# Performance work log

Measured on AMD Instinct MI355X. Metric: run time of the kernel, lower is better.

The kernel has to match this reference:

```python
import jax, jax.numpy as jnp
import numpy as np

N, LATENT, HIDDEN, OUT, B = 65536, 128, 512, 64, 1024
W_WIDTH = 4.0  # LSH bucket width params['w']


def setup_inputs() -> dict:
    key = jax.random.key(0)
    ks = jax.random.split(key, 6)
    return {
        "z": jax.random.normal(ks[0], (N, LATENT), jnp.float32),
        "W1": jax.random.normal(ks[1], (LATENT, HIDDEN), jnp.float32) / np.float32(np.sqrt(LATENT)),
        "b1": jnp.zeros((HIDDEN,), jnp.float32),
        "W2": jax.random.normal(ks[2], (HIDDEN, OUT), jnp.float32) / np.float32(np.sqrt(HIDDEN)),
        "b2": jnp.zeros((OUT,), jnp.float32),
        "a": jax.random.normal(ks[3], (OUT,), jnp.float32),
        "lsh_b": jax.random.uniform(ks[4], (1,), jnp.float32) * W_WIDTH,
    }


def reference(z, W1, b1, W2, b2, a, lsh_b):
    # decoder MLP: latent -> hidden (relu) -> output_dim
    h = jax.nn.relu(z @ W1 + b1)
    x = h @ W2 + b2                                     # [N, OUT]
    # LSH random-projection hash: floor((x.a + b)/w), bucketed mod B
    code = jnp.floor((x @ a + lsh_b[0]) / W_WIDTH)
    bucket = jnp.mod(code.astype(jnp.int32), B)         # [N] segment ids
    # dict-based cluster grouping -> segmented mean per hash bucket
    sums = jax.ops.segment_sum(x, bucket, num_segments=B)                # [B, OUT]
    counts = jax.ops.segment_sum(jnp.ones((x.shape[0],), x.dtype), bucket, num_segments=B)
    means = sums / jnp.maximum(counts, 1.0)[:, None]    # [B, OUT]
    # squared distances point -> every cluster mean (gram trick, no [N,B,OUT] tensor)
    d2 = jnp.maximum(
        jnp.sum(x * x, -1)[:, None] + jnp.sum(means * means, -1)[None, :]
        - 2.0 * (x @ means.T),
        0.0)                                            # [N, B]
    # DEC-style Student-t soft cluster assignment
    q = 1.0 / (1.0 + d2)
    q_s = q / jnp.sum(q, -1, keepdims=True)
    return (q_s, means)
```

## Files before the change

kernel.cpp:

```cpp
#include <hip/hip_runtime.h>
#include <hip/hip_bf16.h>

#define N_PTS   65536
#define LATENT  128
#define HIDDEN  512
#define OUT_D   64
#define NBUCKET 1024
#define ROWS_A  32

typedef __attribute__((ext_vector_type(8))) short frag_ab;
typedef __attribute__((ext_vector_type(4))) float f32x4;

__device__ __forceinline__ short bf16h(float f) {
    union { float f; unsigned u; } c; c.f = f;
    const unsigned r = (c.u + 0x7FFFu + ((c.u >> 16) & 1u)) >> 16;
    return (short)r;
}
__device__ __forceinline__ float bf16tof(short s) {
    union { unsigned u; float f; } c; c.u = ((unsigned)(unsigned short)s) << 16;
    return c.f;
}
__device__ __forceinline__ float fbits(unsigned u) {
    union { unsigned u; float f; } c; c.u = u; return c.f;
}

__global__ __launch_bounds__(256) void prep_weights(
    const float* __restrict__ W1, const float* __restrict__ W2,
    short* __restrict__ w1frag, short* __restrict__ w2frag)
{
    const int tid = blockIdx.x * 256 + threadIdx.x;
    if (tid < 32 * 64 * 4) {
        const int ct = tid >> 8, l = (tid >> 2) & 63, ks = tid & 3;
        const int n = ct * 16 + (l & 15);
        const int k0 = ks * 32 + ((l >> 4) << 3);
        frag_ab hi, lo;
#pragma unroll
        for (int e = 0; e < 8; ++e) {
            const float wv = W1[(size_t)(k0 + e) * HIDDEN + n];
            const short h = bf16h(wv);
            hi[e] = h;
            lo[e] = bf16h(wv - bf16tof(h));
        }
        frag_ab* dst = (frag_ab*)w1frag;
        const int u = ((ct * 64 + l) * 4 + ks) * 2;
        dst[u] = hi; dst[u + 1] = lo;
    } else {
        const int u0 = tid - 32 * 64 * 4;
        const int c = u0 >> 8, ot = (u0 >> 6) & 3, l = u0 & 63;
        const int n = ot * 16 + (l & 15);
        frag_ab hi, lo;
#pragma unroll
        for (int e = 0; e < 8; ++e) {
            const int k = c * 32 + ((e >> 2) << 4) + ((l >> 4) << 2) + (e & 3);
            const float wv = W2[(size_t)k * OUT_D + n];
            const short h = bf16h(wv);
            hi[e] = h;
            lo[e] = bf16h(wv - bf16tof(h));
        }
        frag_ab* dst = (frag_ab*)w2frag;
        const int u = ((c * 4 + ot) * 64 + l) * 2;
        dst[u] = hi; dst[u + 1] = lo;
    }
}

#define WB_UNITS 1728
#define W2L_OFF  1152
#define XP_STRIDE 512
#define BAND_U   5e-4f

__global__ __launch_bounds__(256, 2) void mlp_mfma_kernel(
    const float* __restrict__ z, const short* __restrict__ w1frag,
    const short* __restrict__ w2frag, const float* __restrict__ b1,
    const float* __restrict__ b2, const float* __restrict__ a,
    const float* __restrict__ lsh_b,
    short* __restrict__ xhi, short* __restrict__ xlo,
    float* __restrict__ xnorm_out, int* __restrict__ bucket_out,
    int* __restrict__ wsflag)
{
    __shared__ frag_ab LD[2 * WB_UNITS];
    short* LDs = (short*)LD;
    const int t = threadIdx.x;
    const int l = t & 63, w = t >> 6;
    const int row0 = blockIdx.x * 128 + w * 32;

    frag_ab zh[2][4], zl[2][4];
#pragma unroll
    for (int rg = 0; rg < 2; ++rg)
#pragma unroll
        for (int ks = 0; ks < 4; ++ks) {
            const float* src = z + (size_t)(row0 + rg * 16 + (l & 15)) * LATENT
                             + ks * 32 + ((l >> 4) << 3);
            const float4 p0 = *(const float4*)src;
            const float4 p1 = *(const float4*)(src + 4);
            const float v[8] = {p0.x, p0.y, p0.z, p0.w, p1.x, p1.y, p1.z, p1.w};
#pragma unroll
            for (int e = 0; e < 8; ++e) {
                const short h = bf16h(v[e]);
                zh[rg][ks][e] = h;
                zl[rg][ks][e] = bf16h(v[e] - bf16tof(h));
            }
        }

    f32x4 acc2[2][4];
#pragma unroll
    for (int rg = 0; rg < 2; ++rg)
#pragma unroll
        for (int ot = 0; ot < 4; ++ot) acc2[rg][ot] = (f32x4){0.f, 0.f, 0.f, 0.f};

    const frag_ab* w1g = (const frag_ab*)w1frag;
    const frag_ab* w2g = (const frag_ab*)w2frag;

#pragma unroll
    for (int j = 0; j < 4; ++j) {
        const int i = t + 256 * j;
        LD[(i >> 9) * 576 + ((i >> 3) & 63) * 9 + (i & 7)] = w1g[i];
    }
#pragma unroll
    for (int j = 0; j < 2; ++j) {
        const int i = t + 256 * j;
        LD[W2L_OFF + ((i >> 1) & 63) * 9 + (((i >> 7) << 1) | (i & 1))] = w2g[i];
    }
    __syncthreads();

#pragma unroll 1
    for (int c = 0; c < 16; ++c) {
        const int pb = (c & 1) * WB_UNITS;
        const int sb = WB_UNITS - pb;
        frag_ab st1[4], st2[2];
        if (c < 15) {
#pragma unroll
            for (int j = 0; j < 4; ++j) st1[j] = w1g[(c + 1) * 1024 + t + 256 * j];
#pragma unroll
            for (int j = 0; j < 2; ++j) st2[j] = w2g[(c + 1) * 512 + t + 256 * j];
        }

        f32x4 acc1[2][2];
#pragma unroll
        for (int ct_l = 0; ct_l < 2; ++ct_l) {
            frag_ab bh[4], bl[4];
#pragma unroll
            for (int ks = 0; ks < 4; ++ks) {
                bh[ks] = LD[pb + ct_l * 576 + l * 9 + ks * 2];
                bl[ks] = LD[pb + ct_l * 576 + l * 9 + ks * 2 + 1];
            }
#pragma unroll
            for (int rg = 0; rg < 2; ++rg) {
                f32x4 acc = (f32x4){0.f, 0.f, 0.f, 0.f};
#pragma unroll
                for (int ks = 0; ks < 4; ++ks) {
                    acc = __builtin_amdgcn_mfma_f32_16x16x32_bf16(bh[ks], zh[rg][ks], acc, 0, 0, 0);
                    acc = __builtin_amdgcn_mfma_f32_16x16x32_bf16(bl[ks], zh[rg][ks], acc, 0, 0, 0);
                    acc = __builtin_amdgcn_mfma_f32_16x16x32_bf16(bh[ks], zl[rg][ks], acc, 0, 0, 0);
                }
                acc1[ct_l][rg] = acc;
            }
        }

        float4 b1v[2];
#pragma unroll
        for (int ct_l = 0; ct_l < 2; ++ct_l)
            b1v[ct_l] = *(const float4*)&b1[(c * 2 + ct_l) * 16 + ((l >> 4) << 2)];
        frag_ab ah2[2], al2[2];
#pragma unroll
        for (int rg = 0; rg < 2; ++rg)
#pragma unroll
            for (int e = 0; e < 8; ++e) {
                const int tile = e >> 2, r = e & 3;
                const float bb = (r == 0) ? b1v[tile].x : (r == 1) ? b1v[tile].y
                               : (r == 2) ? b1v[tile].z : b1v[tile].w;
                const float hv = fmaxf(acc1[tile][rg][r] + bb, 0.f);
                const short hh = bf16h(hv);
                ah2[rg][e] = hh;
                al2[rg][e] = bf16h(hv - bf16tof(hh));
            }

#pragma unroll
        for (int ot = 0; ot < 4; ++ot) {
            const frag_ab b2h = LD[pb + W2L_OFF + l * 9 + ot * 2];
            const frag_ab b2l = LD[pb + W2L_OFF + l * 9 + ot * 2 + 1];
#pragma unroll
            for (int rg = 0; rg < 2; ++rg) {
                acc2[rg][ot] = __builtin_amdgcn_mfma_f32_16x16x32_bf16(ah2[rg], b2h, acc2[rg][ot], 0, 0, 0);
                acc2[rg][ot] = __builtin_amdgcn_mfma_f32_16x16x32_bf16(al2[rg], b2h, acc2[rg][ot], 0, 0, 0);
                acc2[rg][ot] = __builtin_amdgcn_mfma_f32_16x16x32_bf16(ah2[rg], b2l, acc2[rg][ot], 0, 0, 0);
            }
        }

        if (c < 15) {
#pragma unroll
            for (int j = 0; j < 4; ++j) {
                const int i = t + 256 * j;
                LD[sb + (i >> 9) * 576 + ((i >> 3) & 63) * 9 + (i & 7)] = st1[j];
            }
#pragma unroll
            for (int j = 0; j < 2; ++j) {
                const int i = t + 256 * j;
                LD[sb + W2L_OFF + ((i >> 1) & 63) * 9 + (((i >> 7) << 1) | (i & 1))] = st2[j];
            }
        }
        __syncthreads();
    }
    __syncthreads();

    float b2v[4], av[4];
#pragma unroll
    for (int ot = 0; ot < 4; ++ot) {
        b2v[ot] = b2[ot * 16 + (l & 15)];
        av[ot]  = a[ot * 16 + (l & 15)];
    }
    const int pbase = w * XP_STRIDE;
    int flagged = 0;
    const float lb = lsh_b[0];
#pragma unroll
    for (int rg = 0; rg < 2; ++rg)
#pragma unroll
        for (int r = 0; r < 4; ++r) {
            float sp = 0.f, np = 0.f;
            const int row_l = rg * 16 + (l >> 4) * 4 + r;
#pragma unroll
            for (int ot = 0; ot < 4; ++ot) {
                const float xv = acc2[rg][ot][r] + b2v[ot];
                sp = fmaf(xv, av[ot], sp);
                np = fmaf(xv, xv, np);
                const int col = ot * 16 + (l & 15);
                const short xh = bf16h(xv);
                LDs[(pbase + row_l * 8 + (col >> 3)) * 8 + (col & 7)] = xh;
                LDs[(pbase + 256 + row_l * 8 + (col >> 3)) * 8 + (col & 7)] = bf16h(xv - bf16tof(xh));
            }
#pragma unroll
            for (int off = 8; off >= 1; off >>= 1) {
                sp += __shfl_xor(sp, off, 16);
                np += __shfl_xor(np, off, 16);
            }
            if ((l & 15) == 0) {
                const int row = row0 + row_l;
                const float v = sp + lb;
                const float u = v * 0.25f;
                const float fl = floorf(u);
                bucket_out[row] = ((int)fl) & (NBUCKET - 1);
                xnorm_out[row] = np;
                const float fr = u - fl;
                if (fr < BAND_U || fr > 1.f - BAND_U) flagged = 1;
            }
        }
    const unsigned long long fb = __ballot(flagged != 0);
    if (l == 0) wsflag[blockIdx.x * 4 + w] = (fb != 0ull) ? 1 : 0;

    frag_ab* xhi8 = (frag_ab*)xhi;
    frag_ab* xlo8 = (frag_ab*)xlo;
#pragma unroll
    for (int j = 0; j < 4; ++j) {
        const int u = l + 64 * j;
        const size_t gidx = (size_t)(row0 + (u >> 3)) * 8 + (u & 7);
        xhi8[gidx] = LD[pbase + u];
        xlo8[gidx] = LD[pbase + 256 + u];
    }
}

__global__ __launch_bounds__(256, 3) void mlp_fixup_kernel(
    const float* __restrict__ z, const float* __restrict__ W1,
    const float* __restrict__ b1, const float* __restrict__ W2,
    const float* __restrict__ b2, const float* __restrict__ a,
    const float* __restrict__ lsh_b, const int* __restrict__ wsflag,
    short* __restrict__ xhi, short* __restrict__ xlo,
    float* __restrict__ xnorm_out, int* __restrict__ bucket_out)
{
    if (wsflag[blockIdx.x] == 0) return;
    __shared__ float zt[ROWS_A][LATENT];
    __shared__ float ht[ROWS_A][256];
    const int t = threadIdx.x;
    const int row0 = blockIdx.x * ROWS_A;

    {
        const float4* z4 = reinterpret_cast<const float4*>(z + (size_t)row0 * LATENT);
        float4* zt4 = reinterpret_cast<float4*>(&zt[0][0]);
#pragma unroll
        for (int i = 0; i < 4; ++i) zt4[t + 256 * i] = z4[t + 256 * i];
    }
    __syncthreads();

    const int tx = t & 63, ty = t >> 6;
    const int txq = t & 31, tyq = t >> 5;

    float acc2[4][2];
#pragma unroll
    for (int i = 0; i < 4; ++i) { acc2[i][0] = 0.f; acc2[i][1] = 0.f; }

    for (int h = 0; h < 2; ++h) {
        float acc1[8][4];
#pragma unroll
        for (int i = 0; i < 8; ++i)
#pragma unroll
            for (int cc = 0; cc < 4; ++cc) acc1[i][cc] = 0.f;

        const int jbase = h * 256 + tx;
#pragma unroll 2
        for (int k = 0; k < LATENT; k += 4) {
            float wv[4][4];
#pragma unroll
            for (int kk = 0; kk < 4; ++kk)
#pragma unroll
                for (int cc = 0; cc < 4; ++cc)
                    wv[kk][cc] = W1[(size_t)(k + kk) * HIDDEN + jbase + 64 * cc];
            float4 zv[8];
#pragma unroll
            for (int i = 0; i < 8; ++i)
                zv[i] = *reinterpret_cast<const float4*>(&zt[ty * 8 + i][k]);
#pragma unroll
            for (int i = 0; i < 8; ++i)
#pragma unroll
                for (int cc = 0; cc < 4; ++cc) {
                    acc1[i][cc] = fmaf(zv[i].x, wv[0][cc], acc1[i][cc]);
                    acc1[i][cc] = fmaf(zv[i].y, wv[1][cc], acc1[i][cc]);
                    acc1[i][cc] = fmaf(zv[i].z, wv[2][cc], acc1[i][cc]);
                    acc1[i][cc] = fmaf(zv[i].w, wv[3][cc], acc1[i][cc]);
                }
        }
        float bb[4];
#pragma unroll
        for (int cc = 0; cc < 4; ++cc) bb[cc] = b1[jbase + 64 * cc];
#pragma unroll
        for (int i = 0; i < 8; ++i)
#pragma unroll
            for (int cc = 0; cc < 4; ++cc)
                ht[ty * 8 + i][tx + 64 * cc] = fmaxf(acc1[i][cc] + bb[cc], 0.f);
        __syncthreads();

#pragma unroll 2
        for (int k = 0; k < 256; k += 4) {
            float w2v[4][2];
#pragma unroll
            for (int kk = 0; kk < 4; ++kk) {
                w2v[kk][0] = W2[(size_t)(h * 256 + k + kk) * OUT_D + txq];
                w2v[kk][1] = W2[(size_t)(h * 256 + k + kk) * OUT_D + txq + 32];
            }
            float4 hv[4];
#pragma unroll
            for (int i = 0; i < 4; ++i)
                hv[i] = *reinterpret_cast<const float4*>(&ht[tyq * 4 + i][k]);
#pragma unroll
            for (int i = 0; i < 4; ++i)
#pragma unroll
                for (int cc = 0; cc < 2; ++cc) {
                    acc2[i][cc] = fmaf(hv[i].x, w2v[0][cc], acc2[i][cc]);
                    acc2[i][cc] = fmaf(hv[i].y, w2v[1][cc], acc2[i][cc]);
                    acc2[i][cc] = fmaf(hv[i].z, w2v[2][cc], acc2[i][cc]);
                    acc2[i][cc] = fmaf(hv[i].w, w2v[3][cc], acc2[i][cc]);
                }
        }
        __syncthreads();
    }

    const float bb0 = b2[txq], bb1 = b2[txq + 32];
    const float a0 = a[txq], a1 = a[txq + 32];
    const float lb = lsh_b[0];
#pragma unroll
    for (int i = 0; i < 4; ++i) {
        const int row = row0 + tyq * 4 + i;
        const float x0 = acc2[i][0] + bb0;
        const float x1 = acc2[i][1] + bb1;
        const short h0 = bf16h(x0), h1 = bf16h(x1);
        xhi[(size_t)row * OUT_D + txq]      = h0;
        xhi[(size_t)row * OUT_D + txq + 32] = h1;
        xlo[(size_t)row * OUT_D + txq]      = bf16h(x0 - bf16tof(h0));
        xlo[(size_t)row * OUT_D + txq + 32] = bf16h(x1 - bf16tof(h1));

        float sa = fmaf(x0, a0, x1 * a1);
        float sn = fmaf(x0, x0, x1 * x1);
#pragma unroll
        for (int off = 16; off >= 1; off >>= 1) {
            sa += __shfl_xor(sa, off, 32);
            sn += __shfl_xor(sn, off, 32);
        }
        if (txq == 0) {
            const float code = floorf((sa + lb) * 0.25f);
            bucket_out[row] = ((int)code) & (NBUCKET - 1);
            xnorm_out[row] = sn;
        }
    }
}

__global__ __launch_bounds__(256) void hist_kernel(
    const int* __restrict__ bucket, int* __restrict__ blockhist,
    float* __restrict__ sums)
{
    __shared__ int h[NBUCKET];
    const int t = threadIdx.x, blk = blockIdx.x;
    for (int i = t; i < NBUCKET; i += 256) h[i] = 0;
    for (int i = t; i < NBUCKET; i += 256) sums[blk * NBUCKET + i] = 0.f;
    __syncthreads();
    const int rbase = blk * 1024;
#pragma unroll
    for (int i = 0; i < 4; ++i)
        atomicAdd(&h[bucket[rbase + i * 256 + t]], 1);
    __syncthreads();
    for (int i = t; i < NBUCKET; i += 256)
        blockhist[blk * NBUCKET + i] = h[i];
}

__global__ __launch_bounds__(1024) void scan_kernel(
    const int* __restrict__ blockhist, int* __restrict__ base,
    int* __restrict__ blockbase)
{
    __shared__ int sc[NBUCKET];
    const int b = threadIdx.x;
    int c = 0;
#pragma unroll 8
    for (int blk = 0; blk < 64; ++blk) c += blockhist[blk * NBUCKET + b];
    sc[b] = c;
    __syncthreads();
    for (int off = 1; off < NBUCKET; off <<= 1) {
        const int add = (b >= off) ? sc[b - off] : 0;
        __syncthreads();
        sc[b] += add;
        __syncthreads();
    }
    const int offset = sc[b] - c;
    base[b] = offset;
    if (b == NBUCKET - 1) base[NBUCKET] = offset + c;
    int run = offset;
#pragma unroll 4
    for (int blk = 0; blk < 64; ++blk) {
        blockbase[blk * NBUCKET + b] = run;
        run += blockhist[blk * NBUCKET + b];
    }
}

__global__ __launch_bounds__(256) void scatter_kernel(
    const int* __restrict__ bucket, const int* __restrict__ blockbase,
    int* __restrict__ order)
{
    __shared__ int lcur[NBUCKET];
    const int t = threadIdx.x, blk = blockIdx.x;
    for (int i = t; i < NBUCKET; i += 256) lcur[i] = 0;
    __syncthreads();
    const int rbase = blk * 1024;
#pragma unroll
    for (int i = 0; i < 4; ++i) {
        const int row = rbase + i * 256 + t;
        const int bk = bucket[row];
        const int r = atomicAdd(&lcur[bk], 1);
        order[blockbase[blk * NBUCKET + bk] + r] = row;
    }
}

__global__ __launch_bounds__(256) void chunksum_kernel(
    const short* __restrict__ xhi, const short* __restrict__ xlo,
    const int* __restrict__ order, const int* __restrict__ bucket,
    float* __restrict__ sums)
{
    const int t = threadIdx.x, lane = t & 63, w = t >> 6;
    const int c = blockIdx.x * 4 + w;
    const int i0 = c * 64;
    const int ordv = order[i0 + lane];
    const int bktv = bucket[ordv];
    float acc = 0.f;
    int cur = __shfl(bktv, 0, 64);
#pragma unroll 8
    for (int j = 0; j < 64; ++j) {
        const int rb = __shfl(ordv, j, 64);
        const int bb = __shfl(bktv, j, 64);
        if (bb != cur) {
            atomicAdd(&sums[(size_t)cur * OUT_D + lane], acc);
            acc = 0.f; cur = bb;
        }
        acc += bf16tof(xhi[(size_t)rb * OUT_D + lane])
             + bf16tof(xlo[(size_t)rb * OUT_D + lane]);
    }
    atomicAdd(&sums[(size_t)cur * OUT_D + lane], acc);
}

__global__ __launch_bounds__(64) void means_kernel(
    const float* __restrict__ sums, const int* __restrict__ base,
    float* __restrict__ means_out, float* __restrict__ mnorm,
    short* __restrict__ bfrag)
{
    const int b = blockIdx.x;
    const int k = threadIdx.x;
    const int cnt = base[b + 1] - base[b];
    const float m = sums[b * OUT_D + k] / fmaxf((float)cnt, 1.0f);
    means_out[b * OUT_D + k] = m;

    const short mh = bf16h(m);
    const short ml = bf16h(m - bf16tof(mh));
    const int tile = b >> 4, col = b & 15;
    const int lane = ((k & 31) >> 3) * 16 + col;
    const int f = (k >> 5) * 2;
    const size_t idx = ((size_t)(tile * 64 + lane) * 4 + f) * 8 + (k & 7);
    bfrag[idx] = mh;
    bfrag[idx + 8] = ml;

    float s = m * m;
#pragma unroll
    for (int off = 32; off >= 1; off >>= 1) s += __shfl_xor(s, off, 64);
    if (k == 0) mnorm[b] = s;
}

__global__ __launch_bounds__(256, 2) void q_kernel(
    const short* __restrict__ xhi, const short* __restrict__ xlo,
    const float* __restrict__ xnorm, const short* __restrict__ bfrag,
    const float* __restrict__ mnorm, float* __restrict__ q_out)
{
    __shared__ float rs_lds[4][2][16];
    const int t = threadIdx.x;
    const int l = t & 63;
    const int w = t >> 6;
    const int row0 = blockIdx.x * 32;
    const int lrow = (l >> 4) * 4;
    const int lcol = l & 15;

    const frag_ab* xh8 = reinterpret_cast<const frag_ab*>(xhi);
    const frag_ab* xl8 = reinterpret_cast<const frag_ab*>(xlo);
    frag_ab ah[2][2], al[2][2];
#pragma unroll
    for (int s = 0; s < 2; ++s)
#pragma unroll
        for (int kh = 0; kh < 2; ++kh) {
            const size_t idx8 = (size_t)(row0 + s * 16 + lcol) * 8 + kh * 4 + (l >> 4);
            ah[s][kh] = xh8[idx8];
            al[s][kh] = xl8[idx8];
        }

    float xn[2][4];
#pragma unroll
    for (int s = 0; s < 2; ++s)
#pragma unroll
        for (int r = 0; r < 4; ++r) xn[s][r] = xnorm[row0 + s * 16 + lrow + r];

    const frag_ab* bf8 = reinterpret_cast<const frag_ab*>(bfrag);
    unsigned qp[2][16][2];
    float rsp[2][4] = {{0.f,0.f,0.f,0.f},{0.f,0.f,0.f,0.f}};

#pragma unroll
    for (int j = 0; j < 16; ++j) {
        const int bt = w + 4 * j;
        const size_t bb = (size_t)(bt * 64 + l) * 4;
        const frag_ab b0h = bf8[bb + 0];
        const frag_ab b0l = bf8[bb + 1];
        const frag_ab b1h = bf8[bb + 2];
        const frag_ab b1l = bf8[bb + 3];
        const float mn = mnorm[bt * 16 + lcol];

#pragma unroll
        for (int s = 0; s < 2; ++s) {
            f32x4 acc = {0.f, 0.f, 0.f, 0.f};
            acc = __builtin_amdgcn_mfma_f32_16x16x32_bf16(ah[s][0], b0h, acc, 0, 0, 0);
            acc = __builtin_amdgcn_mfma_f32_16x16x32_bf16(ah[s][1], b1h, acc, 0, 0, 0);
            acc = __builtin_amdgcn_mfma_f32_16x16x32_bf16(ah[s][0], b0l, acc, 0, 0, 0);
            acc = __builtin_amdgcn_mfma_f32_16x16x32_bf16(ah[s][1], b1l, acc, 0, 0, 0);
            acc = __builtin_amdgcn_mfma_f32_16x16x32_bf16(al[s][0], b0h, acc, 0, 0, 0);
            acc = __builtin_amdgcn_mfma_f32_16x16x32_bf16(al[s][1], b1h, acc, 0, 0, 0);

            float qq[4];
#pragma unroll
            for (int r = 0; r < 4; ++r) {
                const float d2 = fmaxf(fmaf(-2.f, acc[r], xn[s][r] + mn), 0.f);
                qq[r] = __builtin_amdgcn_rcpf(1.f + d2);
                rsp[s][r] += qq[r];
            }
            qp[s][j][0] = ((unsigned)(unsigned short)bf16h(qq[1]) << 16)
                        | (unsigned)(unsigned short)bf16h(qq[0]);
            qp[s][j][1] = ((unsigned)(unsigned short)bf16h(qq[3]) << 16)
                        | (unsigned)(unsigned short)bf16h(qq[2]);
        }
    }

#pragma unroll
    for (int off = 8; off >= 1; off >>= 1)
#pragma unroll
        for (int s = 0; s < 2; ++s)
#pragma unroll
            for (int r = 0; r < 4; ++r) rsp[s][r] += __shfl_xor(rsp[s][r], off, 16);
    if (lcol == 0) {
#pragma unroll
        for (int s = 0; s < 2; ++s)
#pragma unroll
            for (int r = 0; r < 4; ++r) rs_lds[w][s][lrow + r] = rsp[s][r];
    }
    __syncthreads();

    float inv[2][4];
#pragma unroll
    for (int s = 0; s < 2; ++s)
#pragma unroll
        for (int r = 0; r < 4; ++r) {
            const float tot = rs_lds[0][s][lrow + r] + rs_lds[1][s][lrow + r]
                            + rs_lds[2][s][lrow + r] + rs_lds[3][s][lrow + r];
            inv[s][r] = __builtin_amdgcn_rcpf(tot);
        }

#pragma unroll
    for (int j = 0; j < 16; ++j) {
        const int col = (w + 4 * j) * 16 + lcol;
#pragma unroll
        for (int s = 0; s < 2; ++s) {
            const unsigned u0 = qp[s][j][0], u1 = qp[s][j][1];
            const float q0 = fbits(u0 << 16);
            const float q1 = fbits(u0 & 0xFFFF0000u);
            const float q2 = fbits(u1 << 16);
            const float q3 = fbits(u1 & 0xFFFF0000u);
            const size_t rb = (size_t)(row0 + s * 16 + lrow) * NBUCKET + col;
            q_out[rb]               = q0 * inv[s][0];
            q_out[rb + NBUCKET]     = q1 * inv[s][1];
            q_out[rb + 2 * NBUCKET] = q2 * inv[s][2];
            q_out[rb + 3 * NBUCKET] = q3 * inv[s][3];
        }
    }
}

extern "C" void kernel_launch(void* const* d_in, const int* in_sizes, int n_in,
                              void* d_out, int out_size, void* d_ws, size_t ws_size,
                              hipStream_t stream) {
    const float* z    = (const float*)d_in[0];
    const float* W1   = (const float*)d_in[1];
    const float* b1   = (const float*)d_in[2];
    const float* W2   = (const float*)d_in[3];
    const float* b2   = (const float*)d_in[4];
    const float* a    = (const float*)d_in[5];
    const float* lshb = (const float*)d_in[6];

    float* q_out     = (float*)d_out;
    float* means_out = q_out + (size_t)N_PTS * NBUCKET;

    char* ws = (char*)d_ws;
    short* xhi    = (short*)ws;
    short* xlo    = xhi + (size_t)N_PTS * OUT_D;
    short* bfrag  = xlo + (size_t)N_PTS * OUT_D;
    short* w1frag = bfrag + (size_t)64 * 64 * 4 * 8;
    short* w2frag = w1frag + (size_t)32 * 64 * 8 * 8;
    float* xnorm  = (float*)(w2frag + (size_t)16 * 4 * 64 * 2 * 8);
    float* mnorm  = xnorm + N_PTS;
    float* sums   = mnorm + NBUCKET;
    int*   bucket = (int*)(sums + (size_t)NBUCKET * OUT_D);
    int*   order  = bucket + N_PTS;
    int*   blockhist = order + N_PTS;
    int*   blockbase = blockhist + 64 * NBUCKET;
    int*   base      = blockbase + 64 * NBUCKET;
    int*   wsflag    = base + NBUCKET + 1;

    prep_weights<<<48, 256, 0, stream>>>(W1, W2, w1frag, w2frag);
    mlp_mfma_kernel<<<N_PTS / 128, 256, 0, stream>>>(z, w1frag, w2frag, b1, b2, a, lshb,
                                                     xhi, xlo, xnorm, bucket, wsflag);
    mlp_fixup_kernel<<<N_PTS / ROWS_A, 256, 0, stream>>>(z, W1, b1, W2, b2, a, lshb, wsflag,
                                                         xhi, xlo, xnorm, bucket);
    hist_kernel<<<64, 256, 0, stream>>>(bucket, blockhist, sums);
    scan_kernel<<<1, 1024, 0, stream>>>(blockhist, base, blockbase);
    scatter_kernel<<<64, 256, 0, stream>>>(bucket, blockbase, order);
    chunksum_kernel<<<256, 256, 0, stream>>>(xhi, xlo, order, bucket, sums);
    means_kernel<<<NBUCKET, 64, 0, stream>>>(sums, base, means_out, mnorm, bfrag);
    q_kernel<<<N_PTS / 32, 256, 0, stream>>>(xhi, xlo, xnorm, bfrag, mnorm, q_out);
}
```

Before: 230.8 us.

## Stream MLP weight chunks via direct global-to-LDS loads with XOR-swizzled layout

Weight fragments are repacked per chunk into one contiguous XOR-swizzled layout, and the MLP kernel now copies them into LDS with global_load_lds. Previously they went through registers, with padding used to avoid bank conflicts. This frees the staging registers and removes the explicit LDS store pass in the double-buffered loop. The q output stores also switch to nontemporal to avoid polluting the cache with the large output. One risk is async LDS load visibility: correctness relies only on the existing __syncthreads, with no explicit vmcnt wait.

```diff
diff --git a/kernel.cpp b/kernel.cpp
--- a/kernel.cpp
+++ b/kernel.cpp
@@ -26,14 +26,18 @@
 
 __global__ __launch_bounds__(256) void prep_weights(
     const float* __restrict__ W1, const float* __restrict__ W2,
-    short* __restrict__ w1frag, short* __restrict__ w2frag)
+    short* __restrict__ wfrag)
 {
     const int tid = blockIdx.x * 256 + threadIdx.x;
-    if (tid < 32 * 64 * 4) {
-        const int ct = tid >> 8, l = (tid >> 2) & 63, ks = tid & 3;
-        const int n = ct * 16 + (l & 15);
+    const int c = tid / 1536;
+    const int u = tid % 1536;
+    frag_ab hi, lo;
+    if (u < 1024) {
+        const int l = u >> 4, slot = u & 15;
+        const int j = slot ^ (l & 7);
+        const int ct = j >> 3, ks = (j >> 1) & 3, hl = j & 1;
+        const int n = (c * 2 + ct) * 16 + (l & 15);
         const int k0 = ks * 32 + ((l >> 4) << 3);
-        frag_ab hi, lo;
 #pragma unroll
         for (int e = 0; e < 8; ++e) {
             const float wv = W1[(size_t)(k0 + e) * HIDDEN + n];
@@ -41,14 +45,13 @@
             hi[e] = h;
             lo[e] = bf16h(wv - bf16tof(h));
         }
-        frag_ab* dst = (frag_ab*)w1frag;
-        const int u = ((ct * 64 + l) * 4 + ks) * 2;
-        dst[u] = hi; dst[u + 1] = lo;
+        ((frag_ab*)wfrag)[(size_t)c * 1536 + u] = hl ? lo : hi;
     } else {
-        const int u0 = tid - 32 * 64 * 4;
-        const int c = u0 >> 8, ot = (u0 >> 6) & 3, l = u0 & 63;
+        const int u2 = u - 1024;
+        const int l = u2 >> 3, slot = u2 & 7;
+        const int j = slot ^ (l & 7);
+        const int ot = j >> 1, hl = j & 1;
         const int n = ot * 16 + (l & 15);
-        frag_ab hi, lo;
 #pragma unroll
         for (int e = 0; e < 8; ++e) {
             const int k = c * 32 + ((e >> 2) << 4) + ((l >> 4) << 2) + (e & 3);
@@ -57,31 +60,28 @@
             hi[e] = h;
             lo[e] = bf16h(wv - bf16tof(h));
         }
-        frag_ab* dst = (frag_ab*)w2frag;
-        const int u = ((c * 4 + ot) * 64 + l) * 2;
-        dst[u] = hi; dst[u + 1] = lo;
-    }
-}
-
-#define WB_UNITS 1728
-#define W2L_OFF  1152
+        ((frag_ab*)wfrag)[(size_t)c * 1536 + u] = hl ? lo : hi;
+    }
+}
+
 #define XP_STRIDE 512
 #define BAND_U   5e-4f
 
 __global__ __launch_bounds__(256, 2) void mlp_mfma_kernel(
-    const float* __restrict__ z, const short* __restrict__ w1frag,
-    const short* __restrict__ w2frag, const float* __restrict__ b1,
-    const float* __restrict__ b2, const float* __restrict__ a,
-    const float* __restrict__ lsh_b,
+    const float* __restrict__ z, const short* __restrict__ wfrag,
+    const float* __restrict__ b1, const float* __restrict__ b2,
+    const float* __restrict__ a, const float* __restrict__ lsh_b,
     short* __restrict__ xhi, short* __restrict__ xlo,
     float* __restrict__ xnorm_out, int* __restrict__ bucket_out,
     int* __restrict__ wsflag)
 {
-    __shared__ frag_ab LD[2 * WB_UNITS];
+    __shared__ frag_ab LD[3072];
     short* LDs = (short*)LD;
     const int t = threadIdx.x;
     const int l = t & 63, w = t >> 6;
+    const int sw = l & 7;
     const int row0 = blockIdx.x * 128 + w * 32;
+    const frag_ab* wg = (const frag_ab*)wfrag;
 
     frag_ab zh[2][4], zl[2][4];
 #pragma unroll
@@ -107,31 +107,25 @@
 #pragma unroll
         for (int ot = 0; ot < 4; ++ot) acc2[rg][ot] = (f32x4){0.f, 0.f, 0.f, 0.f};
 
-    const frag_ab* w1g = (const frag_ab*)w1frag;
-    const frag_ab* w2g = (const frag_ab*)w2frag;
-
-#pragma unroll
-    for (int j = 0; j < 4; ++j) {
-        const int i = t + 256 * j;
-        LD[(i >> 9) * 576 + ((i >> 3) & 63) * 9 + (i & 7)] = w1g[i];
-    }
-#pragma unroll
-    for (int j = 0; j < 2; ++j) {
-        const int i = t + 256 * j;
-        LD[W2L_OFF + ((i >> 1) & 63) * 9 + (((i >> 7) << 1) | (i & 1))] = w2g[i];
-    }
+#pragma unroll
+    for (int i = 0; i < 6; ++i)
+        __builtin_amdgcn_global_load_lds(
+            (const __attribute__((address_space(1))) void*)(wg + (w * 6 + i) * 64 + l),
+            (__attribute__((address_space(3))) void*)(&LD[(w * 6 + i) * 64]),
+            16, 0, 0);
     __syncthreads();
 
 #pragma unroll 1
     for (int c = 0; c < 16; ++c) {
-        const int pb = (c & 1) * WB_UNITS;
-        const int sb = WB_UNITS - pb;
-        frag_ab st1[4], st2[2];
+        const int pb = (c & 1) * 1536;
+        const int sb = 1536 - pb;
         if (c < 15) {
 #pragma unroll
-            for (int j = 0; j < 4; ++j) st1[j] = w1g[(c + 1) * 1024 + t + 256 * j];
-#pragma unroll
-            for (int j = 0; j < 2; ++j) st2[j] = w2g[(c + 1) * 512 + t + 256 * j];
+            for (int i = 0; i < 6; ++i)
+                __builtin_amdgcn_global_load_lds(
+                    (const __attribute__((address_space(1))) void*)(wg + (size_t)(c + 1) * 1536 + (w * 6 + i) * 64 + l),
+                    (__attribute__((address_space(3))) void*)(&LD[sb + (w * 6 + i) * 64]),
+                    16, 0, 0);
         }
 
         f32x4 acc1[2][2];
@@ -140,8 +134,8 @@
             frag_ab bh[4], bl[4];
 #pragma unroll
             for (int ks = 0; ks < 4; ++ks) {
-                bh[ks] = LD[pb + ct_l * 576 + l * 9 + ks * 2];
-                bl[ks] = LD[pb + ct_l * 576 + l * 9 + ks * 2 + 1];
+                bh[ks] = LD[pb + l * 16 + ct_l * 8 + ((ks * 2) ^ sw)];
+                bl[ks] = LD[pb + l * 16 + ct_l * 8 + ((ks * 2 + 1) ^ sw)];
             }
 #pragma unroll
             for (int rg = 0; rg < 2; ++rg) {
@@ -176,8 +170,8 @@
 
 #pragma unroll
         for (int ot = 0; ot < 4; ++ot) {
-            const frag_ab b2h = LD[pb + W2L_OFF + l * 9 + ot * 2];
-            const frag_ab b2l = LD[pb + W2L_OFF + l * 9 + ot * 2 + 1];
+            const frag_ab b2h = LD[pb + 1024 + l * 8 + ((ot * 2) ^ sw)];
+            const frag_ab b2l = LD[pb + 1024 + l * 8 + ((ot * 2 + 1) ^ sw)];
 #pragma unroll
             for (int rg = 0; rg < 2; ++rg) {
                 acc2[rg][ot] = __builtin_amdgcn_mfma_f32_16x16x32_bf16(ah2[rg], b2h, acc2[rg][ot], 0, 0, 0);
@@ -185,22 +179,8 @@
                 acc2[rg][ot] = __builtin_amdgcn_mfma_f32_16x16x32_bf16(ah2[rg], b2l, acc2[rg][ot], 0, 0, 0);
             }
         }
-
-        if (c < 15) {
-#pragma unroll
-            for (int j = 0; j < 4; ++j) {
-                const int i = t + 256 * j;
-                LD[sb + (i >> 9) * 576 + ((i >> 3) & 63) * 9 + (i & 7)] = st1[j];
-            }
-#pragma unroll
-            for (int j = 0; j < 2; ++j) {
-                const int i = t + 256 * j;
-                LD[sb + W2L_OFF + ((i >> 1) & 63) * 9 + (((i >> 7) << 1) | (i & 1))] = st2[j];
-            }
-        }
         __syncthreads();
     }
-    __syncthreads();
 
     float b2v[4], av[4];
 #pragma unroll
@@ -600,10 +580,10 @@
             const float q2 = fbits(u1 << 16);
             const float q3 = fbits(u1 & 0xFFFF0000u);
             const size_t rb = (size_t)(row0 + s * 16 + lrow) * NBUCKET + col;
-            q_out[rb]               = q0 * inv[s][0];
-            q_out[rb + NBUCKET]     = q1 * inv[s][1];
-            q_out[rb + 2 * NBUCKET] = q2 * inv[s][2];
-            q_out[rb + 3 * NBUCKET] = q3 * inv[s][3];
+            __builtin_nontemporal_store(q0 * inv[s][0], &q_out[rb]);
+            __builtin_nontemporal_store(q1 * inv[s][1], &q_out[rb + NBUCKET]);
+            __builtin_nontemporal_store(q2 * inv[s][2], &q_out[rb + 2 * NBUCKET]);
+            __builtin_nontemporal_store(q3 * inv[s][3], &q_out[rb + 3 * NBUCKET]);
         }
     }
 }
@@ -626,9 +606,8 @@
     short* xhi    = (short*)ws;
     short* xlo    = xhi + (size_t)N_PTS * OUT_D;
     short* bfrag  = xlo + (size_t)N_PTS * OUT_D;
-    short* w1frag = bfrag + (size_t)64 * 64 * 4 * 8;
-    short* w2frag = w1frag + (size_t)32 * 64 * 8 * 8;
-    float* xnorm  = (float*)(w2frag + (size_t)16 * 4 * 64 * 2 * 8);
+    short* wfrag  = bfrag + (size_t)64 * 64 * 4 * 8;
+    float* xnorm  = (float*)(wfrag + (size_t)16 * 1536 * 8);
     float* mnorm  = xnorm + N_PTS;
     float* sums   = mnorm + NBUCKET;
     int*   bucket = (int*)(sums + (size_t)NBUCKET * OUT_D);
@@ -638,8 +617,8 @@
     int*   base      = blockbase + 64 * NBUCKET;
     int*   wsflag    = base + NBUCKET + 1;
 
-    prep_weights<<<48, 256, 0, stream>>>(W1, W2, w1frag, w2frag);
-    mlp_mfma_kernel<<<N_PTS / 128, 256, 0, stream>>>(z, w1frag, w2frag, b1, b2, a, lshb,
+    prep_weights<<<96, 256, 0, stream>>>(W1, W2, wfrag);
+    mlp_mfma_kernel<<<N_PTS / 128, 256, 0, stream>>>(z, wfrag, b1, b2, a, lshb,
                                                      xhi, xlo, xnorm, bucket, wsflag);
     mlp_fixup_kernel<<<N_PTS / ROWS_A, 256, 0, stream>>>(z, W1, b1, W2, b2, a, lshb, wsflag,
                                                          xhi, xlo, xnorm, bucket);
```

After: 231.5 us. About the same (+0.3%).
